# Kernel optimization log

Measured on AMD Instinct MI355X. Metric: run time of the kernel, lower is better.

Reference implementation:

```python
import jax, jax.numpy as jnp
import numpy as np

EMBED_DIM = 512
VIR_HEADS = 8


def _make_buffers():
    # angle: 1/10000**linspace(0,1,embed//H//2), each entry repeated twice (rotary pairs)
    half = EMBED_DIM // VIR_HEADS // 2
    angle = 1.0 / 10000 ** jnp.linspace(0.0, 1.0, half)
    angle = jnp.repeat(angle, 2)  # [head_dim]
    decay = jnp.log(1 - 2 ** (-2 - 5 * jnp.arange(VIR_HEADS, dtype=jnp.float32) / VIR_HEADS))
    return angle.astype(jnp.float32), decay.astype(jnp.float32)


def setup_inputs() -> dict:
    key = jax.random.key(0)
    B, H, N1, N2 = 8, 8, 32, 32
    offsets = jax.random.normal(key, (B, H, N1, N2, 2), dtype=jnp.float32)
    angle, decay = _make_buffers()
    return {"slen": N1 * N2, "offsets": offsets, "angle": angle, "decay": decay}


def reference(slen, offsets, angle, decay):
    B, H, N1, N2, _ = offsets.shape
    idx1 = jnp.arange(N1, dtype=offsets.dtype)
    idx2 = jnp.arange(N2, dtype=offsets.dtype)

    # key-side rotary phases: index_k[i*N2+j] = i + j
    index_k = (idx1[:, None] + idx2[None, :]).reshape(slen)  # [slen]
    phase_k = index_k[:, None] * angle[None, :]               # [slen, D]
    sin_k, cos_k = jnp.sin(phase_k), jnp.cos(phase_k)

    # query-side deformed indices
    index1_q = idx1.reshape(1, 1, N1, 1) + offsets[..., 0]    # [B,H,N1,N2]
    index2_q = idx2.reshape(1, 1, 1, N2) + offsets[..., 1]    # [B,H,N1,N2]
    index_q = (index1_q + index2_q).reshape(B, H, slen, 1)    # [B,H,slen,1]
    phase_q = index_q * angle.reshape(1, 1, 1, -1)            # [B,H,slen,D]
    sin_q, cos_q = jnp.sin(phase_q), jnp.cos(phase_q)

    # L1 distance between deformed query position and each key grid position
    d1 = jnp.abs(index1_q[..., None, None] - idx1.reshape(1, 1, 1, 1, N1, 1))  # [B,H,N1,N2,N1,1]
    d2 = jnp.abs(index2_q[..., None, None] - idx2.reshape(1, 1, 1, 1, 1, N2))  # [B,H,N1,N2,1,N2]
    mask = (d1 + d2).reshape(B, H, slen, slen)
    mask = jnp.exp(mask * decay[None, :, None, None])
    mask = jnp.nan_to_num(mask)
    mask = mask / jnp.sqrt(jnp.sum(mask, axis=-1, keepdims=True))
    return sin_q, cos_q, sin_k, cos_k, mask
```

## Files before the change

kernel.cpp:

```cpp
#include <hip/hip_runtime.h>
#include <math.h>

#define OFF_COSQ  4194304
#define OFF_SINK  8388608
#define OFF_COSK  8454144
#define OFF_MASK  8519680
#define NROWS     65536

typedef float floatx4 __attribute__((ext_vector_type(4)));

__global__ __launch_bounds__(256) void retnet_fused_kernel(
    const float* __restrict__ offsets,
    const float* __restrict__ angle,
    const float* __restrict__ decay,
    float* __restrict__ out)
{
    const int wave = blockIdx.x * 4 + (threadIdx.x >> 6);
    const int lane = threadIdx.x & 63;
    if (wave >= NROWS) return;

    const int bh = wave >> 10;
    const int s  = wave & 1023;
    const int h  = bh & 7;
    const int i  = s >> 5;
    const int j  = s & 31;

    const float off0 = offsets[(wave << 1) + 0];
    const float off1 = offsets[(wave << 1) + 1];
    const float i1q  = (float)i + off0;
    const float i2q  = (float)j + off1;
    const float dec  = decay[h];
    const float ang  = angle[lane];

    {
        float sq, cq;
        __sincosf((i1q + i2q) * ang, &sq, &cq);
        __builtin_nontemporal_store(sq, &out[(size_t)wave * 64 + lane]);
        __builtin_nontemporal_store(cq, &out[OFF_COSQ + (size_t)wave * 64 + lane]);
    }

    if (bh == 0) {
        float sk, ck;
        __sincosf((float)(i + j) * ang, &sk, &ck);
        __builtin_nontemporal_store(sk, &out[OFF_SINK + (size_t)s * 64 + lane]);
        __builtin_nontemporal_store(ck, &out[OFF_COSK + (size_t)s * 64 + lane]);
    }

    float v;
    if (lane < 32) v = __expf(dec * fabsf(i1q - (float)lane));
    else           v = __expf(dec * fabsf(i2q - (float)(lane - 32)));

    float sum = v;
    #pragma unroll
    for (int m = 16; m >= 1; m >>= 1) sum += __shfl_xor(sum, m, 64);
    const float sum1 = __shfl(sum, 0, 64);
    const float sum2 = __shfl(sum, 32, 64);
    const float invnorm = rsqrtf(sum1 * sum2);

    const int jj0 = (lane & 7) * 4;
    float e2a[4];
    #pragma unroll
    for (int c = 0; c < 4; ++c)
        e2a[c] = __expf(dec * fabsf(i2q - (float)(jj0 + c))) * invnorm;

    floatx4* mrow = (floatx4*)(out + OFF_MASK + (size_t)wave * 1024);
    #pragma unroll
    for (int k = 0; k < 4; ++k) {
        const int ii = k * 8 + (lane >> 3);
        const float e1 = __expf(dec * fabsf(i1q - (float)ii));
        floatx4 r;
        r.x = e1 * e2a[0];
        r.y = e1 * e2a[1];
        r.z = e1 * e2a[2];
        r.w = e1 * e2a[3];
        __builtin_nontemporal_store(r, &mrow[k * 64 + lane]);
    }
}

extern "C" void kernel_launch(void* const* d_in, const int* in_sizes, int n_in,
                              void* d_out, int out_size, void* d_ws, size_t ws_size,
                              hipStream_t stream) {
    const float* offsets = (const float*)d_in[1];
    const float* angle   = (const float*)d_in[2];
    const float* decay   = (const float*)d_in[3];
    float* out = (float*)d_out;

    const int blocks = NROWS / 4;
    retnet_fused_kernel<<<blocks, 256, 0, stream>>>(offsets, angle, decay, out);
}
```

Before: 301.3 us.

## Compute mask normalizer via closed-form geometric sums and drop nontemporal stores

Replaces the wave-shuffle reduction of the row sums with a closed-form geometric-series expression evaluated per lane using native exp2. It also reorders the stores so the large mask write comes first, switches from nontemporal to regular stores, loads the two offsets as one float2, and drops the bounds check. This is meant to remove the shuffle latency and cut transcendental work. The closed form may differ slightly numerically near clamped or boundary positions, and regular stores may pollute the cache.

```diff
diff --git a/kernel.cpp b/kernel.cpp
--- a/kernel.cpp
+++ b/kernel.cpp
@@ -9,6 +9,10 @@
 
 typedef float floatx4 __attribute__((ext_vector_type(4)));
 
+__device__ __forceinline__ float hexp2(float x) {
+    return __builtin_amdgcn_exp2f(x);
+}
+
 __global__ __launch_bounds__(256) void retnet_fused_kernel(
     const float* __restrict__ offsets,
     const float* __restrict__ angle,
@@ -17,7 +21,6 @@
 {
     const int wave = blockIdx.x * 4 + (threadIdx.x >> 6);
     const int lane = threadIdx.x & 63;
-    if (wave >= NROWS) return;
 
     const int bh = wave >> 10;
     const int s  = wave & 1023;
@@ -25,55 +28,53 @@
     const int i  = s >> 5;
     const int j  = s & 31;
 
-    const float off0 = offsets[(wave << 1) + 0];
-    const float off1 = offsets[(wave << 1) + 1];
-    const float i1q  = (float)i + off0;
-    const float i2q  = (float)j + off1;
+    const float2 off = *(const float2*)(offsets + (wave << 1));
+    const float i1q  = (float)i + off.x;
+    const float i2q  = (float)j + off.y;
     const float dec  = decay[h];
-    const float ang  = angle[lane];
+    const float L    = dec * 1.44269504089f;
 
+    const float inv1mr = 1.0f / (1.0f - hexp2(L));
+    const float m1 = fminf(fmaxf(floorf(i1q), -1.0f), 31.0f);
+    const float S1 = (hexp2(L * (i1q - m1)) + hexp2(L * (m1 + 1.0f - i1q))
+                    - hexp2(L * (i1q + 1.0f)) - hexp2(L * (32.0f - i1q))) * inv1mr;
+    const float m2 = fminf(fmaxf(floorf(i2q), -1.0f), 31.0f);
+    const float S2 = (hexp2(L * (i2q - m2)) + hexp2(L * (m2 + 1.0f - i2q))
+                    - hexp2(L * (i2q + 1.0f)) - hexp2(L * (32.0f - i2q))) * inv1mr;
+    const float invnorm = rsqrtf(S1 * S2);
+
+    const int jj0 = (lane & 7) * 4;
+    float e2a[4];
+    #pragma unroll
+    for (int c = 0; c < 4; ++c)
+        e2a[c] = hexp2(L * fabsf(i2q - (float)(jj0 + c))) * invnorm;
+
+    floatx4* mrow = (floatx4*)(out + OFF_MASK + (size_t)wave * 1024);
+    #pragma unroll
+    for (int k = 0; k < 4; ++k) {
+        const int ii = k * 8 + (lane >> 3);
+        const float e1 = hexp2(L * fabsf(i1q - (float)ii));
+        floatx4 r;
+        r.x = e1 * e2a[0];
+        r.y = e1 * e2a[1];
+        r.z = e1 * e2a[2];
+        r.w = e1 * e2a[3];
+        mrow[k * 64 + lane] = r;
+    }
+
+    const float ang = angle[lane];
     {
         float sq, cq;
         __sincosf((i1q + i2q) * ang, &sq, &cq);
-        __builtin_nontemporal_store(sq, &out[(size_t)wave * 64 + lane]);
-        __builtin_nontemporal_store(cq, &out[OFF_COSQ + (size_t)wave * 64 + lane]);
+        out[(size_t)wave * 64 + lane] = sq;
+        out[OFF_COSQ + (size_t)wave * 64 + lane] = cq;
     }
 
     if (bh == 0) {
         float sk, ck;
         __sincosf((float)(i + j) * ang, &sk, &ck);
-        __builtin_nontemporal_store(sk, &out[OFF_SINK + (size_t)s * 64 + lane]);
-        __builtin_nontemporal_store(ck, &out[OFF_COSK + (size_t)s * 64 + lane]);
-    }
-
-    float v;
-    if (lane < 32) v = __expf(dec * fabsf(i1q - (float)lane));
-    else           v = __expf(dec * fabsf(i2q - (float)(lane - 32)));
-
-    float sum = v;
-    #pragma unroll
-    for (int m = 16; m >= 1; m >>= 1) sum += __shfl_xor(sum, m, 64);
-    const float sum1 = __shfl(sum, 0, 64);
-    const float sum2 = __shfl(sum, 32, 64);
-    const float invnorm = rsqrtf(sum1 * sum2);
-
-    const int jj0 = (lane & 7) * 4;
-    float e2a[4];
-    #pragma unroll
-    for (int c = 0; c < 4; ++c)
-        e2a[c] = __expf(dec * fabsf(i2q - (float)(jj0 + c))) * invnorm;
-
-    floatx4* mrow = (floatx4*)(out + OFF_MASK + (size_t)wave * 1024);
-    #pragma unroll
-    for (int k = 0; k < 4; ++k) {
-        const int ii = k * 8 + (lane >> 3);
-        const float e1 = __expf(dec * fabsf(i1q - (float)ii));
-        floatx4 r;
-        r.x = e1 * e2a[0];
-        r.y = e1 * e2a[1];
-        r.z = e1 * e2a[2];
-        r.w = e1 * e2a[3];
-        __builtin_nontemporal_store(r, &mrow[k * 64 + lane]);
+        out[OFF_SINK + (size_t)s * 64 + lane] = sk;
+        out[OFF_COSK + (size_t)s * 64 + lane] = ck;
     }
 }
 
```

Measured after the change: 304.4 us. No clear change (+1.0%).
